# Kernel optimization log

Measured on AMD Instinct MI355X. Metric: run time of the kernel, lower is better.

## Reference

```python
import jax, jax.numpy as jnp
import numpy as np

EPS = 1e-8

def setup_inputs() -> dict:
    key = jax.random.key(0)
    k1, k2, k3 = jax.random.split(key, 3)
    B, K, D = 2048, 128, 512
    x = jax.random.normal(k1, (B, D), dtype=jnp.float32)
    centers = jax.random.uniform(k2, (K, D), dtype=jnp.float32)
    Dm = 0.2 * jax.random.uniform(k3, (K, D), dtype=jnp.float32) + 0.9
    return {"x": x, "centers": centers, "D": Dm}

def reference(x, centers, D):
    # Per-class diagonal Mahalanobis distance + GMM log-responsibilities.
    D_abs = jnp.abs(D) + EPS                      # [K, d]
    log_det = jnp.sum(jnp.log(D_abs), axis=1)     # [K]
    det_sf = -0.5 * log_det
    det_scale = jnp.exp(det_sf - jnp.max(det_sf)) # [K]

    diff = x[:, None, :] - centers[None, :, :]    # [B, K, d]
    # diag Sigma_inv: dist_sq = sum_d diff^2 / D_abs
    dist_sq = jnp.einsum('bkd,kd->bk', diff * diff, 1.0 / D_abs)  # [B, K]

    expo = -0.5 * dist_sq
    expo_safe = expo - jnp.max(expo, axis=-1, keepdims=True)
    numer = det_scale[None, :] * jnp.exp(expo_safe)               # [B, K]
    resp = numer / jnp.sum(numer, axis=1, keepdims=True)
    resp_gmm = jnp.log(jnp.clip(resp, 1e-8, None))                # [B, K]

    cluster_assignment = jnp.argmax(resp_gmm, axis=1)             # [B]
    cluster_dist_mat = jnp.sqrt(dist_sq)                          # [B, K]
    cluster_dist = jnp.take_along_axis(
        cluster_dist_mat, cluster_assignment[:, None], axis=1)[:, 0]
    return resp_gmm, cluster_dist
```

## Files before the change

### kernel.cpp

```cpp
#include <hip/hip_runtime.h>
#include <math.h>

#define TB 2048
#define TK 128
#define TD 512
#define BR 4
#define NBLK (TB / BR)
#define NKS 32

typedef _Float16 half8 __attribute__((ext_vector_type(8)));
typedef float f32x4 __attribute__((ext_vector_type(4)));


__global__ __launch_bounds__(128) void prep_kernel(const float* __restrict__ C,
        const float* __restrict__ Dm, _Float16* __restrict__ Wfrag,
        float* __restrict__ off, float* __restrict__ ebuf) {
    __shared__ float sE[2], sL[2];
    const int k = blockIdx.x;
    const int t = threadIdx.x;
    const int ks = t >> 2, lg = t & 3;
    const int d0 = ks * 16 + lg * 4;

    float4 dv = *reinterpret_cast<const float4*>(&Dm[(size_t)k * TD + d0]);
    float4 cv = *reinterpret_cast<const float4*>(&C[(size_t)k * TD + d0]);
    float a0 = fabsf(dv.x) + 1e-8f, a1 = fabsf(dv.y) + 1e-8f;
    float a2 = fabsf(dv.z) + 1e-8f, a3 = fabsf(dv.w) + 1e-8f;
    float i0 = 1.f / a0, i1 = 1.f / a1, i2 = 1.f / a2, i3 = 1.f / a3;
    float c0 = cv.x * i0, c1 = cv.y * i1, c2 = cv.z * i2, c3 = cv.w * i3;

    half8 h;
    h[0] = (_Float16)i0; h[1] = (_Float16)(-2.f * c0);
    h[2] = (_Float16)i1; h[3] = (_Float16)(-2.f * c1);
    h[4] = (_Float16)i2; h[5] = (_Float16)(-2.f * c2);
    h[6] = (_Float16)i3; h[7] = (_Float16)(-2.f * c3);
    *reinterpret_cast<half8*>(
        &Wfrag[(((size_t)(k >> 4) * NKS + ks) * 64 + lg * 16 + (k & 15)) * 8]) = h;

    float es = (cv.x * c0 + cv.y * c1) + (cv.z * c2 + cv.w * c3);
    float ls = logf((a0 * a1) * (a2 * a3));
    #pragma unroll
    for (int m = 1; m <= 32; m <<= 1) {
        es += __shfl_xor(es, m, 64);
        ls += __shfl_xor(ls, m, 64);
    }
    if ((t & 63) == 0) { sE[t >> 6] = es; sL[t >> 6] = ls; }
    __syncthreads();
    if (t == 0) {
        float E = sE[0] + sE[1], L = sL[0] + sL[1];
        off[k] = -0.5f * (E + L);
        ebuf[k] = E;
    }
}

__global__ __launch_bounds__(1024) void gmm_kernel(const float* __restrict__ x,
        const _Float16* __restrict__ Wfrag, const float* __restrict__ off,
        const float* __restrict__ ebuf, float* __restrict__ out) {
    __shared__ __align__(16) _Float16 XAf[NKS * 64 * 8];
    __shared__ __align__(16) float accX[8][64][4];
    __shared__ float red_m[8][BR], red_s[8][BR], red_g[8][BR];
    __shared__ int   red_i[8][BR];
    __shared__ float red_lse[BR];

    const int tid = threadIdx.x;
    const int l = tid & 63;
    const int w = tid >> 6;
    const int kh = w >> 3;
    const int wc = w & 7;
    const int l15 = l & 15;
    const int lg = l >> 4;
    const int b0 = blockIdx.x * BR;
    const int col = wc * 16 + l15;

    #pragma unroll
    for (int i = 0; i < 2; ++i) {
        int rec = tid + i * 1024;
        int ks = rec >> 6;
        int lr = rec & 63;
        int row = lr & 15;
        int lgr = lr >> 4;
        half8 h = (half8){0, 0, 0, 0, 0, 0, 0, 0};
        if (row < BR) {
            int d0 = ks * 16 + lgr * 4;
            float4 v = *reinterpret_cast<const float4*>(
                &x[(size_t)(b0 + row) * TD + d0]);
            h[0] = (_Float16)(v.x * v.x); h[1] = (_Float16)v.x;
            h[2] = (_Float16)(v.y * v.y); h[3] = (_Float16)v.y;
            h[4] = (_Float16)(v.z * v.z); h[5] = (_Float16)v.z;
            h[6] = (_Float16)(v.w * v.w); h[7] = (_Float16)v.w;
        }
        *reinterpret_cast<half8*>(&XAf[(size_t)rec * 8]) = h;
    }
    __syncthreads();

    const half8* wfp = reinterpret_cast<const half8*>(Wfrag)
                       + ((size_t)(wc * NKS + kh * 16) * 64 + l);
    const half8* xap = reinterpret_cast<const half8*>(XAf)
                       + ((size_t)(kh * 16) * 64 + l);
    f32x4 acc0 = (f32x4){0.f, 0.f, 0.f, 0.f};
    f32x4 acc1 = (f32x4){0.f, 0.f, 0.f, 0.f};
    #pragma unroll
    for (int i = 0; i < 16; i += 2) {
        half8 bv0 = wfp[(size_t)i * 64];
        half8 av0 = xap[(size_t)i * 64];
        half8 bv1 = wfp[(size_t)(i + 1) * 64];
        half8 av1 = xap[(size_t)(i + 1) * 64];
        acc0 = __builtin_amdgcn_mfma_f32_16x16x32_f16(av0, bv0, acc0, 0, 0, 0);
        acc1 = __builtin_amdgcn_mfma_f32_16x16x32_f16(av1, bv1, acc1, 0, 0, 0);
    }
    f32x4 acc = acc0 + acc1;

    if (kh == 1) *reinterpret_cast<f32x4*>(&accX[wc][l][0]) = acc;
    __syncthreads();

    float sv[4];
    if (kh == 0) {
        acc += *reinterpret_cast<const f32x4*>(&accX[wc][l][0]);

        const float offc = off[col];
        float bv[4], bg[4], ps[4];
        int bi[4];
        #pragma unroll
        for (int e = 0; e < 4; ++e) {
            sv[e] = fmaf(-0.5f, acc[e], offc);
            bv[e] = sv[e]; bi[e] = col; bg[e] = acc[e];
        }
        #pragma unroll
        for (int msk = 1; msk <= 8; msk <<= 1) {
            #pragma unroll
            for (int e = 0; e < 4; ++e) {
                float ov = __shfl_xor(bv[e], msk, 64);
                int   oi = __shfl_xor(bi[e], msk, 64);
                float og = __shfl_xor(bg[e], msk, 64);
                if (ov > bv[e] || (ov == bv[e] && oi < bi[e])) {
                    bv[e] = ov; bi[e] = oi; bg[e] = og;
                }
            }
        }
        #pragma unroll
        for (int e = 0; e < 4; ++e) ps[e] = expf(sv[e] - bv[e]);
        #pragma unroll
        for (int msk = 1; msk <= 8; msk <<= 1)
            #pragma unroll
            for (int e = 0; e < 4; ++e) ps[e] += __shfl_xor(ps[e], msk, 64);

        if (l == 0) {
            #pragma unroll
            for (int e = 0; e < 4; ++e) {
                red_m[wc][e] = bv[e];
                red_s[wc][e] = ps[e];
                red_i[wc][e] = bi[e];
                red_g[wc][e] = bg[e];
            }
        }
    }
    __syncthreads();

    if (w == 8 && l < BR) {
        const int r = l;
        float M = red_m[0][r];
        #pragma unroll
        for (int w2 = 1; w2 < 8; ++w2) M = fmaxf(M, red_m[w2][r]);
        float S = 0.f;
        #pragma unroll
        for (int w2 = 0; w2 < 8; ++w2) S += red_s[w2][r] * expf(red_m[w2][r] - M);
        red_lse[r] = logf(S) + M;

        float v = red_m[0][r]; int ki = red_i[0][r]; float g = red_g[0][r];
        #pragma unroll
        for (int w2 = 1; w2 < 8; ++w2) {
            float v2 = red_m[w2][r]; int i2 = red_i[w2][r];
            if (v2 > v || (v2 == v && i2 < ki)) { v = v2; ki = i2; g = red_g[w2][r]; }
        }
        out[(size_t)TB * TK + b0 + r] = sqrtf(fmaxf(g + ebuf[ki], 0.f));
    }
    __syncthreads();

    if (kh == 0 && lg == 0) {
        const float LOGC = -18.420680743952367f;
        #pragma unroll
        for (int e = 0; e < 4; ++e) {
            out[(size_t)(b0 + e) * TK + col] = fmaxf(sv[e] - red_lse[e], LOGC);
        }
    }
}

extern "C" void kernel_launch(void* const* d_in, const int* in_sizes, int n_in,
                              void* d_out, int out_size, void* d_ws, size_t ws_size,
                              hipStream_t stream) {
    const float* x  = (const float*)d_in[0];
    const float* C  = (const float*)d_in[1];
    const float* Dm = (const float*)d_in[2];
    float* out = (float*)d_out;

    _Float16* Wfrag = (_Float16*)d_ws;
    float* off  = (float*)((char*)d_ws + (size_t)TK * 2 * TD * 2);
    float* ebuf = off + TK;

    prep_kernel<<<TK, 128, 0, stream>>>(C, Dm, Wfrag, off, ebuf);
    gmm_kernel<<<NBLK, 1024, 0, stream>>>(x, Wfrag, off, ebuf, out);
}
```

Baseline: 20.52 us.

## Precompute x MFMA fragments in prep kernel and double rows per block

The squaring and fp16 packing of x move into the prep kernel, which writes pre-swizzled A fragments to a global workspace. The GMM kernel then streams A straight from global memory instead of staging it in LDS. Each block now handles 8 batch rows instead of 4, so half as many blocks re-read the shared W fragments, and launch bounds request two blocks per CU. In exchange, the padded fp16 fragment buffer adds a global write and read of several megabytes plus extra prep blocks.

Measured after the change: 19.69 us. 4.0% less time.

```diff
diff --git a/kernel.cpp b/kernel.cpp
--- a/kernel.cpp
+++ b/kernel.cpp
@@ -4,58 +4,86 @@
 #define TB 2048
 #define TK 128
 #define TD 512
-#define BR 4
-#define NBLK (TB / BR)
+#define BR 8
+#define NTILE (TB / BR)
 #define NKS 32
 
 typedef _Float16 half8 __attribute__((ext_vector_type(8)));
 typedef float f32x4 __attribute__((ext_vector_type(4)));
 
 
-__global__ __launch_bounds__(128) void prep_kernel(const float* __restrict__ C,
-        const float* __restrict__ Dm, _Float16* __restrict__ Wfrag,
+__global__ __launch_bounds__(128) void prep_kernel(const float* __restrict__ x,
+        const float* __restrict__ C, const float* __restrict__ Dm,
+        _Float16* __restrict__ Wfrag, _Float16* __restrict__ XF,
         float* __restrict__ off, float* __restrict__ ebuf) {
     __shared__ float sE[2], sL[2];
-    const int k = blockIdx.x;
+    const int bid = blockIdx.x;
     const int t = threadIdx.x;
-    const int ks = t >> 2, lg = t & 3;
-    const int d0 = ks * 16 + lg * 4;
-
-    float4 dv = *reinterpret_cast<const float4*>(&Dm[(size_t)k * TD + d0]);
-    float4 cv = *reinterpret_cast<const float4*>(&C[(size_t)k * TD + d0]);
-    float a0 = fabsf(dv.x) + 1e-8f, a1 = fabsf(dv.y) + 1e-8f;
-    float a2 = fabsf(dv.z) + 1e-8f, a3 = fabsf(dv.w) + 1e-8f;
-    float i0 = 1.f / a0, i1 = 1.f / a1, i2 = 1.f / a2, i3 = 1.f / a3;
-    float c0 = cv.x * i0, c1 = cv.y * i1, c2 = cv.z * i2, c3 = cv.w * i3;
-
-    half8 h;
-    h[0] = (_Float16)i0; h[1] = (_Float16)(-2.f * c0);
-    h[2] = (_Float16)i1; h[3] = (_Float16)(-2.f * c1);
-    h[4] = (_Float16)i2; h[5] = (_Float16)(-2.f * c2);
-    h[6] = (_Float16)i3; h[7] = (_Float16)(-2.f * c3);
-    *reinterpret_cast<half8*>(
-        &Wfrag[(((size_t)(k >> 4) * NKS + ks) * 64 + lg * 16 + (k & 15)) * 8]) = h;
-
-    float es = (cv.x * c0 + cv.y * c1) + (cv.z * c2 + cv.w * c3);
-    float ls = logf((a0 * a1) * (a2 * a3));
-    #pragma unroll
-    for (int m = 1; m <= 32; m <<= 1) {
-        es += __shfl_xor(es, m, 64);
-        ls += __shfl_xor(ls, m, 64);
-    }
-    if ((t & 63) == 0) { sE[t >> 6] = es; sL[t >> 6] = ls; }
-    __syncthreads();
-    if (t == 0) {
-        float E = sE[0] + sE[1], L = sL[0] + sL[1];
-        off[k] = -0.5f * (E + L);
-        ebuf[k] = E;
+
+    if (bid < TK) {
+        const int k = bid;
+        const int ks = t >> 2, lg = t & 3;
+        const int d0 = ks * 16 + lg * 4;
+
+        float4 dv = *reinterpret_cast<const float4*>(&Dm[(size_t)k * TD + d0]);
+        float4 cv = *reinterpret_cast<const float4*>(&C[(size_t)k * TD + d0]);
+        float a0 = fabsf(dv.x) + 1e-8f, a1 = fabsf(dv.y) + 1e-8f;
+        float a2 = fabsf(dv.z) + 1e-8f, a3 = fabsf(dv.w) + 1e-8f;
+        float i0 = 1.f / a0, i1 = 1.f / a1, i2 = 1.f / a2, i3 = 1.f / a3;
+        float c0 = cv.x * i0, c1 = cv.y * i1, c2 = cv.z * i2, c3 = cv.w * i3;
+
+        half8 h;
+        h[0] = (_Float16)i0; h[1] = (_Float16)(-2.f * c0);
+        h[2] = (_Float16)i1; h[3] = (_Float16)(-2.f * c1);
+        h[4] = (_Float16)i2; h[5] = (_Float16)(-2.f * c2);
+        h[6] = (_Float16)i3; h[7] = (_Float16)(-2.f * c3);
+        *reinterpret_cast<half8*>(
+            &Wfrag[(((size_t)(k >> 4) * NKS + ks) * 64 + lg * 16 + (k & 15)) * 8]) = h;
+
+        float es = (cv.x * c0 + cv.y * c1) + (cv.z * c2 + cv.w * c3);
+        float ls = logf((a0 * a1) * (a2 * a3));
+        #pragma unroll
+        for (int m = 1; m <= 32; m <<= 1) {
+            es += __shfl_xor(es, m, 64);
+            ls += __shfl_xor(ls, m, 64);
+        }
+        if ((t & 63) == 0) { sE[t >> 6] = es; sL[t >> 6] = ls; }
+        __syncthreads();
+        if (t == 0) {
+            float E = sE[0] + sE[1], L = sL[0] + sL[1];
+            off[k] = -0.5f * (E + L);
+            ebuf[k] = E;
+        }
+    } else {
+        const int tile = bid - TK;
+        const int b0 = tile * BR;
+        #pragma unroll
+        for (int i = 0; i < 16; ++i) {
+            int rec = t + i * 128;
+            int ks = rec >> 6;
+            int ln = rec & 63;
+            int row = ln & 15;
+            int lgr = ln >> 4;
+            half8 h = (half8){0, 0, 0, 0, 0, 0, 0, 0};
+            if (row < BR) {
+                int d0 = ks * 16 + lgr * 4;
+                float4 v = *reinterpret_cast<const float4*>(
+                    &x[(size_t)(b0 + row) * TD + d0]);
+                h[0] = (_Float16)(v.x * v.x); h[1] = (_Float16)v.x;
+                h[2] = (_Float16)(v.y * v.y); h[3] = (_Float16)v.y;
+                h[4] = (_Float16)(v.z * v.z); h[5] = (_Float16)v.z;
+                h[6] = (_Float16)(v.w * v.w); h[7] = (_Float16)v.w;
+            }
+            *reinterpret_cast<half8*>(
+                &XF[((size_t)(tile * NKS + ks) * 64 + ln) * 8]) = h;
+        }
     }
 }
 
-__global__ __launch_bounds__(1024) void gmm_kernel(const float* __restrict__ x,
-        const _Float16* __restrict__ Wfrag, const float* __restrict__ off,
-        const float* __restrict__ ebuf, float* __restrict__ out) {
-    __shared__ __align__(16) _Float16 XAf[NKS * 64 * 8];
+__global__ __launch_bounds__(1024, 2) void gmm_kernel(
+        const _Float16* __restrict__ XF, const _Float16* __restrict__ Wfrag,
+        const float* __restrict__ off, const float* __restrict__ ebuf,
+        float* __restrict__ out) {
     __shared__ __align__(16) float accX[8][64][4];
     __shared__ float red_m[8][BR], red_s[8][BR], red_g[8][BR];
     __shared__ int   red_i[8][BR];
@@ -71,39 +99,19 @@
     const int b0 = blockIdx.x * BR;
     const int col = wc * 16 + l15;
 
-    #pragma unroll
-    for (int i = 0; i < 2; ++i) {
-        int rec = tid + i * 1024;
-        int ks = rec >> 6;
-        int lr = rec & 63;
-        int row = lr & 15;
-        int lgr = lr >> 4;
-        half8 h = (half8){0, 0, 0, 0, 0, 0, 0, 0};
-        if (row < BR) {
-            int d0 = ks * 16 + lgr * 4;
-            float4 v = *reinterpret_cast<const float4*>(
-                &x[(size_t)(b0 + row) * TD + d0]);
-            h[0] = (_Float16)(v.x * v.x); h[1] = (_Float16)v.x;
-            h[2] = (_Float16)(v.y * v.y); h[3] = (_Float16)v.y;
-            h[4] = (_Float16)(v.z * v.z); h[5] = (_Float16)v.z;
-            h[6] = (_Float16)(v.w * v.w); h[7] = (_Float16)v.w;
-        }
-        *reinterpret_cast<half8*>(&XAf[(size_t)rec * 8]) = h;
-    }
-    __syncthreads();
-
-    const half8* wfp = reinterpret_cast<const half8*>(Wfrag)
-                       + ((size_t)(wc * NKS + kh * 16) * 64 + l);
-    const half8* xap = reinterpret_cast<const half8*>(XAf)
-                       + ((size_t)(kh * 16) * 64 + l);
+    const half8* ap = reinterpret_cast<const half8*>(XF)
+                      + ((size_t)(blockIdx.x * NKS + kh * 16) * 64 + l);
+    const half8* bp = reinterpret_cast<const half8*>(Wfrag)
+                      + ((size_t)(wc * NKS + kh * 16) * 64 + l);
+
     f32x4 acc0 = (f32x4){0.f, 0.f, 0.f, 0.f};
     f32x4 acc1 = (f32x4){0.f, 0.f, 0.f, 0.f};
     #pragma unroll
     for (int i = 0; i < 16; i += 2) {
-        half8 bv0 = wfp[(size_t)i * 64];
-        half8 av0 = xap[(size_t)i * 64];
-        half8 bv1 = wfp[(size_t)(i + 1) * 64];
-        half8 av1 = xap[(size_t)(i + 1) * 64];
+        half8 av0 = ap[(size_t)i * 64];
+        half8 bv0 = bp[(size_t)i * 64];
+        half8 av1 = ap[(size_t)(i + 1) * 64];
+        half8 bv1 = bp[(size_t)(i + 1) * 64];
         acc0 = __builtin_amdgcn_mfma_f32_16x16x32_f16(av0, bv0, acc0, 0, 0, 0);
         acc1 = __builtin_amdgcn_mfma_f32_16x16x32_f16(av1, bv1, acc1, 0, 0, 0);
     }
@@ -143,13 +151,14 @@
             #pragma unroll
             for (int e = 0; e < 4; ++e) ps[e] += __shfl_xor(ps[e], msk, 64);
 
-        if (l == 0) {
+        if (l15 == 0 && lg < 2) {
             #pragma unroll
             for (int e = 0; e < 4; ++e) {
-                red_m[wc][e] = bv[e];
-                red_s[wc][e] = ps[e];
-                red_i[wc][e] = bi[e];
-                red_g[wc][e] = bg[e];
+                int r = lg * 4 + e;
+                red_m[wc][r] = bv[e];
+                red_s[wc][r] = ps[e];
+                red_i[wc][r] = bi[e];
+                red_g[wc][r] = bg[e];
             }
         }
     }
@@ -175,11 +184,12 @@
     }
     __syncthreads();
 
-    if (kh == 0 && lg == 0) {
+    if (kh == 0 && lg < 2) {
         const float LOGC = -18.420680743952367f;
         #pragma unroll
         for (int e = 0; e < 4; ++e) {
-            out[(size_t)(b0 + e) * TK + col] = fmaxf(sv[e] - red_lse[e], LOGC);
+            int r = lg * 4 + e;
+            out[(size_t)(b0 + r) * TK + col] = fmaxf(sv[e] - red_lse[r], LOGC);
         }
     }
 }
@@ -195,7 +205,8 @@
     _Float16* Wfrag = (_Float16*)d_ws;
     float* off  = (float*)((char*)d_ws + (size_t)TK * 2 * TD * 2);
     float* ebuf = off + TK;
-
-    prep_kernel<<<TK, 128, 0, stream>>>(C, Dm, Wfrag, off, ebuf);
-    gmm_kernel<<<NBLK, 1024, 0, stream>>>(x, Wfrag, off, ebuf, out);
+    _Float16* XF = (_Float16*)((char*)d_ws + (1 << 20));
+
+    prep_kernel<<<TK + NTILE, 128, 0, stream>>>(x, C, Dm, Wfrag, XF, off, ebuf);
+    gmm_kernel<<<NTILE, 1024, 0, stream>>>(XF, Wfrag, off, ebuf, out);
 }
```
